# Optimization experiments

Hardware: AMD Instinct MI355X
Metric: run time of the kernel (lower is better)

## Reference

```python
import jax, jax.numpy as jnp
import numpy as np

N = 40000   # entities
R = 200     # relations
T = 250000  # train edges (one direction)
E = 2 * T + N  # fwd + reverse + self-loops
D0, D = 100, 200   # init_emb_size, embedding_dim (= gc1_emb_size)
C, K = 128, 5      # conv channels, kernel size
B = 2048           # query batch
EPS = 1e-5


def setup_inputs() -> dict:
    key = jax.random.key(0)
    ks = jax.random.split(key, 24)
    def nrm(k, shape, s=0.05):
        return jax.random.normal(k, shape, jnp.float32) * s
    def bnp(k, dim):  # [gamma, beta, running_mean, running_var] stacked -> [4, dim]
        g = 1.0 + nrm(k, (dim,))
        b = nrm(jax.random.fold_in(k, 1), (dim,))
        m = nrm(jax.random.fold_in(k, 2), (dim,))
        v = 1.0 + 0.1 * jax.random.uniform(jax.random.fold_in(k, 3), (dim,), jnp.float32)
        return jnp.stack([g, b, m, v])
    inp = dict(
        src=jax.random.randint(ks[0], (E,), 0, N),
        dst=jax.random.randint(ks[1], (E,), 0, N),
        all_edge_type=jax.random.randint(ks[2], (E,), 0, R + 1),
        e1=jax.random.randint(ks[3], (B, 1), 0, N),
        rel=jax.random.randint(ks[4], (B, 1), 0, R),
        entity_id=jnp.arange(N),
        emb_e_w=nrm(ks[5], (N, D0), 0.1).at[0].set(0.0),   # padding_idx=0
        emb_rel_w=nrm(ks[6], (R, D), 0.1).at[0].set(0.0),
        w2=nrm(ks[7], (D0, D)), b2=nrm(ks[8], (D,)),
        alpha2=nrm(ks[9], (R + 1, 1)).at[0].set(0.0),
        w3=nrm(ks[10], (D, D)), b3=nrm(ks[11], (D,)),
        alpha3=nrm(ks[12], (R + 1, 1)).at[0].set(0.0),
        bn3=bnp(ks[13], D), bn4=bnp(ks[14], D),
        bn0=bnp(ks[15], 2), bn1=bnp(ks[16], C), bn2=bnp(ks[17], D),
        conv_w=nrm(ks[18], (C, 2, K)), conv_b=nrm(ks[19], (C,)),
        fc_w=nrm(ks[20], (D, D * C), 0.01), fc_b=nrm(ks[21], (D,)),
    )
    return inp


def _bn(x, p):  # eval-mode BatchNorm1d over last dim; p: [4, dim]
    g, b, m, v = p[0], p[1], p[2], p[3]
    return g * (x - m) * jax.lax.rsqrt(v + EPS) + b


def _bn_ch(x, p):  # x: [B, C, L]; normalize over channel dim
    g, b, m, v = (p[i][None, :, None] for i in range(4))
    return g * (x - m) * jax.lax.rsqrt(v + EPS) + b


def _gcn(x, w, b, alpha, src, dst, alp_types, alp_types_t, n):
    feats = x @ w                                   # [N, out]
    alp = alpha[alp_types] + alpha[alp_types_t]     # [E, 1]
    out = jax.ops.segment_sum(feats[src] * alp, dst, num_segments=n)
    return out + b


def reference(src, dst, all_edge_type, e1, rel, entity_id,
              emb_e_w, emb_rel_w, w2, b2, alpha2, w3, b3, alpha3,
              bn3, bn4, bn0, bn1, bn2, conv_w, conv_b, fc_w, fc_b):
    n = entity_id.shape[0]
    t = (all_edge_type.shape[0] - n) // 2
    # transpose edge types: [reverse, forward, self-loops]
    types_t = jnp.concatenate([all_edge_type[t:2 * t], all_edge_type[:t], all_edge_type[2 * t:]])

    x = emb_e_w[entity_id]                                   # [N, D0]
    x = _gcn(x, w2, b2, alpha2, src, dst, all_edge_type, types_t, n)
    x = jnp.tanh(_bn(x, bn3))                                # dropout: eval -> identity
    x = _gcn(x, w3, b3, alpha3, src, dst, all_edge_type, types_t, n)
    x = jnp.tanh(_bn(x, bn4))                                # final_bn + final_act
    e_all = x                                                # [N, D]

    e1_emb = e_all[e1]                                       # [B, 1, D]
    rel_emb = emb_rel_w[rel]                                 # [B, 1, D]
    h = jnp.concatenate([e1_emb, rel_emb], axis=1)           # [B, 2, D]
    h = _bn_ch(h, bn0)
    h = jax.lax.conv_general_dilated(h, conv_w, (1,), [(K // 2, K // 2)],
                                     dimension_numbers=('NCH', 'OIH', 'NCH'))
    h = h + conv_b[None, :, None]                            # [B, C, D]
    h = jax.nn.relu(_bn_ch(h, bn1))
    h = h.reshape(h.shape[0], -1)                            # [B, C*D]
    h = h @ fc_w.T + fc_b                                    # [B, D]
    h = jax.nn.relu(_bn(h, bn2))
    return jax.nn.sigmoid(h @ e_all.T)                       # [B, N]
```

## Files before the change

kernel.cpp:

```cpp
#include <hip/hip_runtime.h>
#include <math.h>

#define NENT 40000
#define NTE  250000
#define NE   540000
#define DIM0 100
#define DIM  200
#define CCH  128
#define BQ   2048
#define FCK  25600
#define EPSB 1e-5f
#define KPAD 224
#define EMBS 104
#define NSPLIT 32
#define KSEG 800

typedef float f32x4 __attribute__((ext_vector_type(4)));
typedef _Float16 h8 __attribute__((ext_vector_type(8)));
typedef _Float16 h4 __attribute__((ext_vector_type(4)));

#if defined(__has_builtin)
#if __has_builtin(__builtin_amdgcn_global_load_lds)
#define HAVE_GLL 1
#endif
#endif

__device__ __forceinline__ void gload_lds16(const void* g, void* l) {
#ifdef HAVE_GLL
    __builtin_amdgcn_global_load_lds((const __attribute__((address_space(1))) unsigned int*)g,
                                     (__attribute__((address_space(3))) unsigned int*)l, 16, 0, 0);
#else
    *(uint4*)l = *(const uint4*)g;
#endif
}

__global__ void k_hist(const int* __restrict__ dst, int* __restrict__ deg) {
    int e = blockIdx.x * 256 + threadIdx.x;
    if (e < NE) atomicAdd(&deg[dst[e]], 1);
}

__global__ __launch_bounds__(1024) void k_scan(const int* __restrict__ deg,
        int* __restrict__ rowptr, int* __restrict__ cursor) {
    __shared__ int sums[1024];
    int t = threadIdx.x;
    int base = t * 40;
    int local[40];
    int s = 0;
    #pragma unroll
    for (int i = 0; i < 40; i++) {
        int idx = base + i;
        int v = (idx < NENT) ? deg[idx] : 0;
        local[i] = s;
        s += v;
    }
    sums[t] = s;
    __syncthreads();
    #pragma unroll
    for (int off = 1; off < 1024; off <<= 1) {
        int add = (t >= off) ? sums[t - off] : 0;
        __syncthreads();
        sums[t] += add;
        __syncthreads();
    }
    int prefix = (t == 0) ? 0 : sums[t - 1];
    #pragma unroll
    for (int i = 0; i < 40; i++) {
        int idx = base + i;
        if (idx < NENT) {
            int p = prefix + local[i];
            rowptr[idx] = p;
            cursor[idx] = p;
        }
    }
    if (t == 1023) rowptr[NENT] = prefix + s;
}

__global__ void k_scatter(const int* __restrict__ src, const int* __restrict__ dst,
                          const int* __restrict__ aet, const float* __restrict__ a2t,
                          const float* __restrict__ a3t, int* __restrict__ cursor,
                          int* __restrict__ ssrc, float* __restrict__ sa1,
                          float* __restrict__ sa2) {
    int e = blockIdx.x * 256 + threadIdx.x;
    if (e >= NE) return;
    int tt = (e < NTE) ? e + NTE : (e < 2 * NTE ? e - NTE : e);
    int t0 = aet[e], t1 = aet[tt];
    int pos = atomicAdd(&cursor[dst[e]], 1);
    ssrc[pos] = src[e];
    sa1[pos] = a2t[t0] + a2t[t1];
    sa2[pos] = a3t[t0] + a3t[t1];
}

template<int NL, int NPADL, int SS, int OS>
__global__ __launch_bounds__(256) void k_agg_raw(const int* __restrict__ rowptr,
        const int* __restrict__ ssrc, const float* __restrict__ sa,
        const _Float16* __restrict__ srcd, _Float16* __restrict__ outd) {
    int w = threadIdx.x >> 6, l = threadIdx.x & 63;
    int row = blockIdx.x * 4 + w;
    int beg = rowptr[row], end = rowptr[row + 1];
    bool act = l < NL;
    int col = l * 4;
    float sx = 0.f, sy = 0.f, sz = 0.f, sw = 0.f;
    int i = beg;
    for (; i + 4 <= end; i += 4) {
        int i0 = ssrc[i], i1 = ssrc[i + 1], i2 = ssrc[i + 2], i3 = ssrc[i + 3];
        float a0 = sa[i], a1 = sa[i + 1], a2 = sa[i + 2], a3 = sa[i + 3];
        if (act) {
            h4 v0 = *(const h4*)(srcd + (long)i0 * SS + col);
            h4 v1 = *(const h4*)(srcd + (long)i1 * SS + col);
            h4 v2 = *(const h4*)(srcd + (long)i2 * SS + col);
            h4 v3 = *(const h4*)(srcd + (long)i3 * SS + col);
            sx += a0 * (float)v0[0] + a1 * (float)v1[0] + a2 * (float)v2[0] + a3 * (float)v3[0];
            sy += a0 * (float)v0[1] + a1 * (float)v1[1] + a2 * (float)v2[1] + a3 * (float)v3[1];
            sz += a0 * (float)v0[2] + a1 * (float)v1[2] + a2 * (float)v2[2] + a3 * (float)v3[2];
            sw += a0 * (float)v0[3] + a1 * (float)v1[3] + a2 * (float)v2[3] + a3 * (float)v3[3];
        }
    }
    for (; i < end; i++) {
        int i0 = ssrc[i];
        float a0 = sa[i];
        if (act) {
            h4 v0 = *(const h4*)(srcd + (long)i0 * SS + col);
            sx += a0 * (float)v0[0]; sy += a0 * (float)v0[1];
            sz += a0 * (float)v0[2]; sw += a0 * (float)v0[3];
        }
    }
    if (act) {
        h4 o = { (_Float16)sx, (_Float16)sy, (_Float16)sz, (_Float16)sw };
        *(h4*)(outd + (long)row * OS + col) = o;
    } else if (l < NPADL) {
        h4 z = { (_Float16)0.f, (_Float16)0.f, (_Float16)0.f, (_Float16)0.f };
        *(h4*)(outd + (long)row * OS + col) = z;
    }
}

__global__ void k_pack_emb(const float* __restrict__ emb, const int* __restrict__ ent,
                           _Float16* __restrict__ o) {
    long i = (long)blockIdx.x * 256 + threadIdx.x;
    if (i >= (long)NENT * 13) return;
    long m = i / 13;
    int k0 = (int)(i % 13) * 8;
    h8 h = {};
    const float* p = emb + (long)ent[m] * DIM0 + k0;
    #pragma unroll
    for (int j = 0; j < 8; j++)
        if (k0 + j < DIM0) h[j] = (_Float16)p[j];
    *(h8*)(o + m * EMBS + k0) = h;
}

__global__ void k_pack_B16(const float* __restrict__ w, _Float16* __restrict__ bf,
                           int kin, int kpad, int nrows) {
    int i = blockIdx.x * 256 + threadIdx.x;
    if (i >= nrows * kpad) return;
    int k = i % kpad, n = i / kpad;
    bf[i] = (k < kin && n < DIM) ? (_Float16)w[(long)k * DIM + n] : (_Float16)0.f;
}

__global__ void k_hq(const int* __restrict__ e1, const int* __restrict__ rel,
                     const _Float16* __restrict__ ef, const float* __restrict__ embrel,
                     const float* __restrict__ bn0, float* __restrict__ hq) {
    int i = blockIdx.x * 256 + threadIdx.x;
    if (i >= BQ * 2 * DIM) return;
    int d = i % DIM, c = (i / DIM) & 1, b = i / (2 * DIM);
    float val = (c == 0) ? (float)ef[(long)e1[b] * KPAD + d]
                         : embrel[(long)rel[b] * DIM + d];
    float g = bn0[c], be = bn0[2 + c], m = bn0[4 + c], v = bn0[6 + c];
    hq[i] = g * (val - m) * rsqrtf(v + EPSB) + be;
}

__global__ void k_pack_fcw(const float* __restrict__ w, _Float16* __restrict__ wf) {
    long i = (long)blockIdx.x * 256 + threadIdx.x;
    if (i >= (long)208 * (FCK / 8)) return;
    int n = (int)(i / (FCK / 8));
    long k0 = (i % (FCK / 8)) * 8;
    h8 h = {};
    if (n < DIM) {
        const float* p = w + (long)n * FCK + k0;
        #pragma unroll
        for (int j = 0; j < 8; j++) h[j] = (_Float16)p[j];
    }
    *(h8*)(wf + (long)n * FCK + k0) = h;
}

template<int NT>
__global__ __launch_bounds__(256) void k_gemm16f(
        const _Float16* __restrict__ A, const _Float16* __restrict__ B,
        const float* __restrict__ bias, const float* __restrict__ bn,
        _Float16* __restrict__ C, int kpad, int ostride) {
    int w = threadIdx.x >> 6, l = threadIdx.x & 63;
    long m0 = (long)blockIdx.x * 64 + w * 16;
    long arow = m0 + (l & 15);
    int kg = (l >> 4) * 8;
    const _Float16* ap = A + arow * kpad + kg;
    f32x4 acc[NT];
    #pragma unroll
    for (int i = 0; i < NT; i++) acc[i] = (f32x4){0.f, 0.f, 0.f, 0.f};
    for (int kb = 0; kb < kpad; kb += 32) {
        h8 a = *(const h8*)(ap + kb);
        #pragma unroll
        for (int nt = 0; nt < NT; nt++) {
            h8 b = *(const h8*)(B + (long)(nt * 16 + (l & 15)) * kpad + kb + kg);
            acc[nt] = __builtin_amdgcn_mfma_f32_16x16x32_f16(a, b, acc[nt], 0, 0, 0);
        }
    }
    long rowo = m0 + (l >> 4) * 4;
    #pragma unroll
    for (int nt = 0; nt < NT; nt++) {
        int col = nt * 16 + (l & 15);
        if (col < ostride) {
            _Float16 vals[4];
            if (col < DIM) {
                float g = bn[col], be = bn[DIM + col], m = bn[2 * DIM + col],
                      v = bn[3 * DIM + col], bb = bias[col];
                float sc = g * rsqrtf(v + EPSB);
                #pragma unroll
                for (int rr = 0; rr < 4; rr++)
                    vals[rr] = (_Float16)tanhf(sc * (acc[nt][rr] + bb - m) + be);
            } else {
                #pragma unroll
                for (int rr = 0; rr < 4; rr++) vals[rr] = (_Float16)0.f;
            }
            #pragma unroll
            for (int rr = 0; rr < 4; rr++)
                C[(rowo + rr) * ostride + col] = vals[rr];
        }
    }
}

__global__ __launch_bounds__(256) void k_conv2(const float* __restrict__ hq,
        const float* __restrict__ convw, const float* __restrict__ convb,
        const float* __restrict__ bn1, _Float16* __restrict__ hc) {
    __shared__ float hql[400];
    __shared__ float cwl[1280];
    __shared__ float scs[128], shs[128];
    int bl = blockIdx.x;
    int t = threadIdx.x;
    long b = bl;
    for (int i = t; i < 400; i += 256) hql[i] = hq[b * 400 + i];
    for (int i = t; i < 1280; i += 256) cwl[i] = convw[i];
    if (t < 128) {
        float g = bn1[t], be = bn1[CCH + t], m = bn1[2 * CCH + t], v = bn1[3 * CCH + t];
        float s = g * rsqrtf(v + EPSB);
        scs[t] = s;
        shs[t] = be - m * s + s * convb[t];
    }
    __syncthreads();
    int c = t >> 1, half = t & 1, p0 = half * 100;
    float cw[10];
    #pragma unroll
    for (int k = 0; k < 10; k++) cw[k] = cwl[c * 10 + k];
    float sc_ = scs[c], sh_ = shs[c];
    long obase = (long)bl * FCK + c * DIM + p0;
    for (int pc = 0; pc < 100; pc += 4) {
        float w0[8], w1[8];
        #pragma unroll
        for (int j = 0; j < 8; j++) {
            int pp = p0 + pc - 2 + j;
            bool ok = (pp >= 0 && pp < DIM);
            w0[j] = ok ? hql[pp] : 0.f;
            w1[j] = ok ? hql[DIM + pp] : 0.f;
        }
        h4 o;
        #pragma unroll
        for (int j = 0; j < 4; j++) {
            float s = 0.f;
            #pragma unroll
            for (int k = 0; k < 5; k++) s += w0[j + k] * cw[k] + w1[j + k] * cw[5 + k];
            o[j] = (_Float16)fmaxf(sc_ * s + sh_, 0.f);
        }
        *(h4*)&hc[obase + pc] = o;
    }
}

__global__ __launch_bounds__(256) void k_fc2(
        const _Float16* __restrict__ A, const _Float16* __restrict__ B,
        float* __restrict__ fcsum) {
    __shared__ __align__(16) _Float16 ldsB[2][6656];
    int bid = blockIdx.y * 8 + blockIdx.x;
    int wsw = (bid & 7) * 128 + (bid >> 3);
    int mb = wsw & 31, split = wsw >> 5;
    int t = threadIdx.x;
    int w = t >> 6, l = t & 63;
    int kbase = split * KSEG;
    long arow = mb * 64 + w * 16 + (l & 15);
    int kg = (l >> 4) * 8;
    const _Float16* ahp = A + arow * FCK + kbase + kg;

    #pragma unroll
    for (int i = 0; i < 4; i++) {
        int u = i * 256 + t;
        if (u < 832) {
            int r = u >> 2, kc = u & 3;
            gload_lds16(B + (long)r * FCK + kbase + kc * 8, &ldsB[0][u * 8]);
        }
    }
    h8 aN = *(const h8*)(ahp);

    f32x4 acc[13];
    #pragma unroll
    for (int i = 0; i < 13; i++) acc[i] = (f32x4){0.f, 0.f, 0.f, 0.f};

    int buf = 0;
    for (int ks = 0; ks < 25; ks++) {
        __syncthreads();
        if (ks + 1 < 25) {
            int knext = kbase + (ks + 1) * 32;
            #pragma unroll
            for (int i = 0; i < 4; i++) {
                int u = i * 256 + t;
                if (u < 832) {
                    int r = u >> 2, kc = u & 3;
                    gload_lds16(B + (long)r * FCK + knext + kc * 8, &ldsB[buf ^ 1][u * 8]);
                }
            }
        }
        h8 aC = aN;
        if (ks + 1 < 25) aN = *(const h8*)(ahp + (ks + 1) * 32);
        const _Float16* b_base = &ldsB[buf][(l & 15) * 32 + kg];
        #pragma unroll
        for (int nt = 0; nt < 13; nt++) {
            h8 b = *(const h8*)(b_base + nt * 512);
            acc[nt] = __builtin_amdgcn_mfma_f32_16x16x32_f16(aC, b, acc[nt], 0, 0, 0);
        }
        buf ^= 1;
    }
    long rowo = mb * 64 + w * 16 + (l >> 4) * 4;
    #pragma unroll
    for (int nt = 0; nt < 13; nt++) {
        int col = nt * 16 + (l & 15);
        if (col < DIM) {
            #pragma unroll
            for (int rr = 0; rr < 4; rr++)
                unsafeAtomicAdd(&fcsum[(rowo + rr) * DIM + col], acc[nt][rr]);
        }
    }
}

__global__ void k_fcreduce(const float* __restrict__ fcsum, const float* __restrict__ fcb,
                           const float* __restrict__ bn2, _Float16* __restrict__ h3) {
    int i = blockIdx.x * 256 + threadIdx.x;
    if (i >= BQ * KPAD) return;
    int j = i % KPAD, b = i / KPAD;
    _Float16 o = (_Float16)0.f;
    if (j < DIM) {
        float s = fcsum[(long)b * DIM + j] + fcb[j];
        float g = bn2[j], be = bn2[DIM + j], m = bn2[2 * DIM + j], v = bn2[3 * DIM + j];
        s = g * (s - m) * rsqrtf(v + EPSB) + be;
        o = (_Float16)fmaxf(s, 0.f);
    }
    h3[i] = o;
}

__global__ __launch_bounds__(256) void k_mfma_final(
        const _Float16* __restrict__ A, const _Float16* __restrict__ B,
        float* __restrict__ out) {
    __shared__ float tl[4][32][68];
    int bid = blockIdx.y * 8 + blockIdx.x;
    int wsw = (bid & 7) * 625 + (bid >> 3);
    int mbb = wsw & 7, nbb = wsw >> 3;
    int w = threadIdx.x >> 6, l = threadIdx.x & 63;
    int n0 = nbb * 64;
    int m0 = mbb * 256 + w * 64;
    int lr = l & 15;
    int kb = (l >> 4) * 8;
    const _Float16* aph = A + (long)(m0 + lr) * KPAD + kb;
    const _Float16* bph = B + (long)(n0 + lr) * KPAD + kb;
    h8 ac[4], bc[4], an[4], bn_[4];
    #pragma unroll
    for (int x = 0; x < 4; x++) {
        ac[x] = *(const h8*)(aph + (long)x * 16 * KPAD);
        bc[x] = *(const h8*)(bph + (long)x * 16 * KPAD);
    }
    f32x4 acc[4][4];
    #pragma unroll
    for (int i = 0; i < 4; i++)
        #pragma unroll
        for (int j = 0; j < 4; j++) acc[i][j] = (f32x4){0.f, 0.f, 0.f, 0.f};
    for (int kt = 0; kt < 7; kt++) {
        int ko = kt * 32 + 32;
        if (kt < 6) {
            #pragma unroll
            for (int x = 0; x < 4; x++) {
                an[x]  = *(const h8*)(aph + (long)x * 16 * KPAD + ko);
                bn_[x] = *(const h8*)(bph + (long)x * 16 * KPAD + ko);
            }
        }
        #pragma unroll
        for (int mt = 0; mt < 4; mt++)
            #pragma unroll
            for (int nt = 0; nt < 4; nt++)
                acc[mt][nt] = __builtin_amdgcn_mfma_f32_16x16x32_f16(ac[mt], bc[nt], acc[mt][nt], 0, 0, 0);
        if (kt < 6) {
            #pragma unroll
            for (int x = 0; x < 4; x++) { ac[x] = an[x]; bc[x] = bn_[x]; }
        }
    }
    #pragma unroll
    for (int hh = 0; hh < 2; hh++) {
        #pragma unroll
        for (int mt2 = 0; mt2 < 2; mt2++) {
            int mt = hh * 2 + mt2;
            #pragma unroll
            for (int nt = 0; nt < 4; nt++)
                #pragma unroll
                for (int r = 0; r < 4; r++)
                    tl[w][mt2 * 16 + (l >> 4) * 4 + r][nt * 16 + lr] = acc[mt][nt][r];
        }
        #pragma unroll
        for (int i = 0; i < 8; i++) {
            int rr = i * 4 + (l >> 4);
            f32x4 v = *(const f32x4*)&tl[w][rr][lr * 4];
            f32x4 o;
            o.x = __builtin_amdgcn_rcpf(1.f + __expf(-v.x));
            o.y = __builtin_amdgcn_rcpf(1.f + __expf(-v.y));
            o.z = __builtin_amdgcn_rcpf(1.f + __expf(-v.z));
            o.w = __builtin_amdgcn_rcpf(1.f + __expf(-v.w));
            long row = m0 + hh * 32 + rr;
            __builtin_nontemporal_store(o, (f32x4*)&out[row * NENT + n0 + lr * 4]);
        }
    }
}

extern "C" void kernel_launch(void* const* d_in, const int* in_sizes, int n_in,
                              void* d_out, int out_size, void* d_ws, size_t ws_size,
                              hipStream_t stream) {
    (void)in_sizes; (void)n_in; (void)out_size; (void)ws_size;
    const int* src      = (const int*)d_in[0];
    const int* dst      = (const int*)d_in[1];
    const int* aet      = (const int*)d_in[2];
    const int* e1       = (const int*)d_in[3];
    const int* rel      = (const int*)d_in[4];
    const int* entity   = (const int*)d_in[5];
    const float* emb_e  = (const float*)d_in[6];
    const float* embrel = (const float*)d_in[7];
    const float* w2     = (const float*)d_in[8];
    const float* b2     = (const float*)d_in[9];
    const float* alpha2 = (const float*)d_in[10];
    const float* w3     = (const float*)d_in[11];
    const float* b3     = (const float*)d_in[12];
    const float* alpha3 = (const float*)d_in[13];
    const float* bn3    = (const float*)d_in[14];
    const float* bn4    = (const float*)d_in[15];
    const float* bn0    = (const float*)d_in[16];
    const float* bn1    = (const float*)d_in[17];
    const float* bn2    = (const float*)d_in[18];
    const float* convw  = (const float*)d_in[19];
    const float* convb  = (const float*)d_in[20];
    const float* fcw    = (const float*)d_in[21];
    const float* fcb    = (const float*)d_in[22];
    float* out = (float*)d_out;
    float* ws = (float*)d_ws;

    _Float16* emb16 = (_Float16*)ws;
    _Float16* aggE  = (_Float16*)(ws + 3000000);
    _Float16* x1_f  = (_Float16*)(ws + 6000000);
    _Float16* aggX  = (_Float16*)(ws + 11000000);
    _Float16* e_f   = (_Float16*)(ws + 16000000);
    _Float16* fcw_f = (_Float16*)(ws + 21000000);
    _Float16* hc_f  = (_Float16*)(ws + 24000000);
    int*   deg    = (int*)(ws + 51000000);
    int*   rowptr = (int*)(ws + 51050000);
    int*   cursor = (int*)(ws + 51100000);
    int*   ssrc   = (int*)(ws + 51200000);
    float* sa1    = ws + 51800000;
    float* sa2    = ws + 52400000;
    float* fcsum  = ws + 53000000;
    float* hq     = ws + 53500000;
    _Float16* h3_f  = (_Float16*)(ws + 54400000);
    _Float16* w2t_f = (_Float16*)(ws + 54700000);
    _Float16* w3t_f = (_Float16*)(ws + 54750000);

    hipMemsetAsync(deg, 0, NENT * 4, stream);
    k_hist<<<(NE + 255) / 256, 256, 0, stream>>>(dst, deg);
    k_scan<<<1, 1024, 0, stream>>>(deg, rowptr, cursor);
    k_scatter<<<(NE + 255) / 256, 256, 0, stream>>>(src, dst, aet, alpha2, alpha3,
                                                    cursor, ssrc, sa1, sa2);

    k_pack_emb<<<(NENT * 13 + 255) / 256, 256, 0, stream>>>(emb_e, entity, emb16);
    k_pack_B16<<<(208 * 128 + 255) / 256, 256, 0, stream>>>(w2, w2t_f, DIM0, 128, 208);
    k_pack_B16<<<(224 * KPAD + 255) / 256, 256, 0, stream>>>(w3, w3t_f, DIM, KPAD, 224);

    k_agg_raw<26, 32, EMBS, 128><<<NENT / 4, 256, 0, stream>>>(rowptr, ssrc, sa1,
                                                               emb16, aggE);
    k_gemm16f<13><<<NENT / 64, 256, 0, stream>>>(aggE, w2t_f, b2, bn3, x1_f, 128, DIM);

    k_agg_raw<50, 56, DIM, KPAD><<<NENT / 4, 256, 0, stream>>>(rowptr, ssrc, sa2,
                                                               x1_f, aggX);
    k_gemm16f<14><<<NENT / 64, 256, 0, stream>>>(aggX, w3t_f, b3, bn4, e_f, KPAD, KPAD);

    k_hq<<<(BQ * 2 * DIM + 255) / 256, 256, 0, stream>>>(e1, rel, e_f, embrel, bn0, hq);
    k_pack_fcw<<<(int)(((long)208 * (FCK / 8) + 255) / 256), 256, 0, stream>>>(fcw, fcw_f);

    hipMemsetAsync(fcsum, 0, (size_t)BQ * DIM * 4, stream);
    k_conv2<<<BQ, 256, 0, stream>>>(hq, convw, convb, bn1, hc_f);
    k_fc2<<<dim3(8, 128), 256, 0, stream>>>(hc_f, fcw_f, fcsum);
    k_fcreduce<<<(BQ * KPAD + 255) / 256, 256, 0, stream>>>(fcsum, fcb, bn2, h3_f);

    k_mfma_final<<<dim3(8, NENT / 64), 256, 0, stream>>>(h3_f, e_f, out);
}
```

Measured before the change: 543.9 us.

## Fuse conv1d+BN+ReLU into FC split-K GEMM, computing A tiles on the fly

Removes the separate conv kernel that wrote the 2048x25600 fp16 conv output (about 100MB) and re-read it in the FC GEMM. The FC kernel now computes each 64x32 A tile directly from the fp16 query embeddings held in registers, writes it to LDS, and stages B through registers instead of async global-to-LDS loads. The query input is also stored as fp16. In exchange, conv arithmetic is recomputed inside the GEMM loop, each step adds a second barrier, and the B double-buffer is replaced by register prefetching, which may lower overlap.

```diff
diff --git a/kernel.cpp b/kernel.cpp
--- a/kernel.cpp
+++ b/kernel.cpp
@@ -12,27 +12,10 @@
 #define EPSB 1e-5f
 #define KPAD 224
 #define EMBS 104
-#define NSPLIT 32
-#define KSEG 800
 
 typedef float f32x4 __attribute__((ext_vector_type(4)));
 typedef _Float16 h8 __attribute__((ext_vector_type(8)));
 typedef _Float16 h4 __attribute__((ext_vector_type(4)));
-
-#if defined(__has_builtin)
-#if __has_builtin(__builtin_amdgcn_global_load_lds)
-#define HAVE_GLL 1
-#endif
-#endif
-
-__device__ __forceinline__ void gload_lds16(const void* g, void* l) {
-#ifdef HAVE_GLL
-    __builtin_amdgcn_global_load_lds((const __attribute__((address_space(1))) unsigned int*)g,
-                                     (__attribute__((address_space(3))) unsigned int*)l, 16, 0, 0);
-#else
-    *(uint4*)l = *(const uint4*)g;
-#endif
-}
 
 __global__ void k_hist(const int* __restrict__ dst, int* __restrict__ deg) {
     int e = blockIdx.x * 256 + threadIdx.x;
@@ -155,16 +138,16 @@
     bf[i] = (k < kin && n < DIM) ? (_Float16)w[(long)k * DIM + n] : (_Float16)0.f;
 }
 
-__global__ void k_hq(const int* __restrict__ e1, const int* __restrict__ rel,
-                     const _Float16* __restrict__ ef, const float* __restrict__ embrel,
-                     const float* __restrict__ bn0, float* __restrict__ hq) {
+__global__ void k_hq16(const int* __restrict__ e1, const int* __restrict__ rel,
+                       const _Float16* __restrict__ ef, const float* __restrict__ embrel,
+                       const float* __restrict__ bn0, _Float16* __restrict__ hq) {
     int i = blockIdx.x * 256 + threadIdx.x;
     if (i >= BQ * 2 * DIM) return;
     int d = i % DIM, c = (i / DIM) & 1, b = i / (2 * DIM);
     float val = (c == 0) ? (float)ef[(long)e1[b] * KPAD + d]
                          : embrel[(long)rel[b] * DIM + d];
     float g = bn0[c], be = bn0[2 + c], m = bn0[4 + c], v = bn0[6 + c];
-    hq[i] = g * (val - m) * rsqrtf(v + EPSB) + be;
+    hq[i] = (_Float16)(g * (val - m) * rsqrtf(v + EPSB) + be);
 }
 
 __global__ void k_pack_fcw(const float* __restrict__ w, _Float16* __restrict__ wf) {
@@ -226,102 +209,111 @@
     }
 }
 
-__global__ __launch_bounds__(256) void k_conv2(const float* __restrict__ hq,
-        const float* __restrict__ convw, const float* __restrict__ convb,
-        const float* __restrict__ bn1, _Float16* __restrict__ hc) {
-    __shared__ float hql[400];
-    __shared__ float cwl[1280];
-    __shared__ float scs[128], shs[128];
-    int bl = blockIdx.x;
-    int t = threadIdx.x;
-    long b = bl;
-    for (int i = t; i < 400; i += 256) hql[i] = hq[b * 400 + i];
-    for (int i = t; i < 1280; i += 256) cwl[i] = convw[i];
-    if (t < 128) {
-        float g = bn1[t], be = bn1[CCH + t], m = bn1[2 * CCH + t], v = bn1[3 * CCH + t];
-        float s = g * rsqrtf(v + EPSB);
-        scs[t] = s;
-        shs[t] = be - m * s + s * convb[t];
-    }
-    __syncthreads();
-    int c = t >> 1, half = t & 1, p0 = half * 100;
-    float cw[10];
-    #pragma unroll
-    for (int k = 0; k < 10; k++) cw[k] = cwl[c * 10 + k];
-    float sc_ = scs[c], sh_ = shs[c];
-    long obase = (long)bl * FCK + c * DIM + p0;
-    for (int pc = 0; pc < 100; pc += 4) {
-        float w0[8], w1[8];
-        #pragma unroll
-        for (int j = 0; j < 8; j++) {
-            int pp = p0 + pc - 2 + j;
-            bool ok = (pp >= 0 && pp < DIM);
-            w0[j] = ok ? hql[pp] : 0.f;
-            w1[j] = ok ? hql[DIM + pp] : 0.f;
-        }
-        h4 o;
-        #pragma unroll
-        for (int j = 0; j < 4; j++) {
-            float s = 0.f;
-            #pragma unroll
-            for (int k = 0; k < 5; k++) s += w0[j + k] * cw[k] + w1[j + k] * cw[5 + k];
-            o[j] = (_Float16)fmaxf(sc_ * s + sh_, 0.f);
-        }
-        *(h4*)&hc[obase + pc] = o;
-    }
-}
-
-__global__ __launch_bounds__(256) void k_fc2(
-        const _Float16* __restrict__ A, const _Float16* __restrict__ B,
-        float* __restrict__ fcsum) {
-    __shared__ __align__(16) _Float16 ldsB[2][6656];
+__global__ __launch_bounds__(256) void k_convfc(
+        const _Float16* __restrict__ hq16, const float* __restrict__ convw,
+        const float* __restrict__ convb, const float* __restrict__ bn1,
+        const _Float16* __restrict__ B, float* __restrict__ fcsum) {
+    __shared__ _Float16 ldsA[64][40];
+    __shared__ _Float16 ldsB[208][40];
+    __shared__ float cwl[4][12];
     int bid = blockIdx.y * 8 + blockIdx.x;
     int wsw = (bid & 7) * 128 + (bid >> 3);
     int mb = wsw & 31, split = wsw >> 5;
     int t = threadIdx.x;
     int w = t >> 6, l = t & 63;
-    int kbase = split * KSEG;
-    long arow = mb * 64 + w * 16 + (l & 15);
-    int kg = (l >> 4) * 8;
-    const _Float16* ahp = A + arow * FCK + kbase + kg;
-
-    #pragma unroll
-    for (int i = 0; i < 4; i++) {
-        int u = i * 256 + t;
-        if (u < 832) {
-            int r = u >> 2, kc = u & 3;
-            gload_lds16(B + (long)r * FCK + kbase + kc * 8, &ldsB[0][u * 8]);
-        }
-    }
-    h8 aN = *(const h8*)(ahp);
+    int kbase = split * 800;
+    int c0 = split * 4;
+    if (t < 40) cwl[t / 10][t % 10] = convw[(c0 + t / 10) * 10 + t % 10];
+    if (t < 4) {
+        int c = c0 + t;
+        float g = bn1[c], be = bn1[CCH + c], m = bn1[2 * CCH + c], v = bn1[3 * CCH + c];
+        float s = g * rsqrtf(v + EPSB);
+        cwl[t][10] = s;
+        cwl[t][11] = be - m * s + s * convb[c];
+    }
+    __syncthreads();
+
+    int r = t >> 2, q = t & 3;
+    const _Float16* hrow = hq16 + (long)(mb * 64 + r) * 400;
+
+    h8 z = {};
+    h8 v0a, v1a, v2a, v0b, v1b, v2b;
+    {
+        int p = q * 8;
+        v0a = (p >= 8) ? *(const h8*)(hrow + p - 8) : z;
+        v1a = *(const h8*)(hrow + p);
+        v2a = (p + 8 < DIM) ? *(const h8*)(hrow + p + 8) : z;
+        v0b = (p >= 8) ? *(const h8*)(hrow + DIM + p - 8) : z;
+        v1b = *(const h8*)(hrow + DIM + p);
+        v2b = (p + 8 < DIM) ? *(const h8*)(hrow + DIM + p + 8) : z;
+    }
+    h8 bR[4];
+    #pragma unroll
+    for (int i2 = 0; i2 < 4; i2++) {
+        int u = i2 * 256 + t;
+        bR[i2] = (u < 832) ? *(const h8*)(B + (long)(u >> 2) * FCK + kbase + (u & 3) * 8) : z;
+    }
 
     f32x4 acc[13];
     #pragma unroll
     for (int i = 0; i < 13; i++) acc[i] = (f32x4){0.f, 0.f, 0.f, 0.f};
 
-    int buf = 0;
     for (int ks = 0; ks < 25; ks++) {
+        int off = ks * 32 + q * 8;
+        int cl = off / 200;
+        float cwv[12];
+        #pragma unroll
+        for (int k2 = 0; k2 < 12; k2++) cwv[k2] = cwl[cl][k2];
+        float wa[12], wb[12];
+        wa[0] = (float)v0a[6]; wa[1] = (float)v0a[7];
+        wb[0] = (float)v0b[6]; wb[1] = (float)v0b[7];
+        #pragma unroll
+        for (int m2 = 0; m2 < 8; m2++) {
+            wa[2 + m2] = (float)v1a[m2];
+            wb[2 + m2] = (float)v1b[m2];
+        }
+        wa[10] = (float)v2a[0]; wa[11] = (float)v2a[1];
+        wb[10] = (float)v2b[0]; wb[11] = (float)v2b[1];
+        h8 aOut;
+        #pragma unroll
+        for (int j = 0; j < 8; j++) {
+            float s = 0.f;
+            #pragma unroll
+            for (int kk = 0; kk < 5; kk++)
+                s += wa[j + kk] * cwv[kk] + wb[j + kk] * cwv[5 + kk];
+            aOut[j] = (_Float16)fmaxf(cwv[10] * s + cwv[11], 0.f);
+        }
+        *(h8*)&ldsA[r][q * 8] = aOut;
+        #pragma unroll
+        for (int i2 = 0; i2 < 4; i2++) {
+            int u = i2 * 256 + t;
+            if (u < 832) *(h8*)&ldsB[u >> 2][(u & 3) * 8] = bR[i2];
+        }
         __syncthreads();
         if (ks + 1 < 25) {
+            int off1 = (ks + 1) * 32 + q * 8;
+            int cl1 = off1 / 200;
+            int p1 = off1 - cl1 * 200;
+            v0a = (p1 >= 8) ? *(const h8*)(hrow + p1 - 8) : z;
+            v1a = *(const h8*)(hrow + p1);
+            v2a = (p1 + 8 < DIM) ? *(const h8*)(hrow + p1 + 8) : z;
+            v0b = (p1 >= 8) ? *(const h8*)(hrow + DIM + p1 - 8) : z;
+            v1b = *(const h8*)(hrow + DIM + p1);
+            v2b = (p1 + 8 < DIM) ? *(const h8*)(hrow + DIM + p1 + 8) : z;
             int knext = kbase + (ks + 1) * 32;
             #pragma unroll
-            for (int i = 0; i < 4; i++) {
-                int u = i * 256 + t;
-                if (u < 832) {
-                    int r = u >> 2, kc = u & 3;
-                    gload_lds16(B + (long)r * FCK + knext + kc * 8, &ldsB[buf ^ 1][u * 8]);
-                }
+            for (int i2 = 0; i2 < 4; i2++) {
+                int u = i2 * 256 + t;
+                if (u < 832) bR[i2] = *(const h8*)(B + (long)(u >> 2) * FCK + knext + (u & 3) * 8);
             }
         }
-        h8 aC = aN;
-        if (ks + 1 < 25) aN = *(const h8*)(ahp + (ks + 1) * 32);
-        const _Float16* b_base = &ldsB[buf][(l & 15) * 32 + kg];
+        h8 a = *(const h8*)&ldsA[w * 16 + (l & 15)][(l >> 4) * 8];
         #pragma unroll
         for (int nt = 0; nt < 13; nt++) {
-            h8 b = *(const h8*)(b_base + nt * 512);
-            acc[nt] = __builtin_amdgcn_mfma_f32_16x16x32_f16(aC, b, acc[nt], 0, 0, 0);
-        }
-        buf ^= 1;
+            h8 b = *(const h8*)&ldsB[nt * 16 + (l & 15)][(l >> 4) * 8];
+            acc[nt] = __builtin_amdgcn_mfma_f32_16x16x32_f16(a, b, acc[nt], 0, 0, 0);
+        }
+        __syncthreads();
     }
     long rowo = mb * 64 + w * 16 + (l >> 4) * 4;
     #pragma unroll
@@ -456,7 +448,7 @@
     _Float16* aggX  = (_Float16*)(ws + 11000000);
     _Float16* e_f   = (_Float16*)(ws + 16000000);
     _Float16* fcw_f = (_Float16*)(ws + 21000000);
-    _Float16* hc_f  = (_Float16*)(ws + 24000000);
+    _Float16* hq16  = (_Float16*)(ws + 24000000);
     int*   deg    = (int*)(ws + 51000000);
     int*   rowptr = (int*)(ws + 51050000);
     int*   cursor = (int*)(ws + 51100000);
@@ -464,7 +456,6 @@
     float* sa1    = ws + 51800000;
     float* sa2    = ws + 52400000;
     float* fcsum  = ws + 53000000;
-    float* hq     = ws + 53500000;
     _Float16* h3_f  = (_Float16*)(ws + 54400000);
     _Float16* w2t_f = (_Float16*)(ws + 54700000);
     _Float16* w3t_f = (_Float16*)(ws + 54750000);
@@ -487,12 +478,11 @@
                                                                x1_f, aggX);
     k_gemm16f<14><<<NENT / 64, 256, 0, stream>>>(aggX, w3t_f, b3, bn4, e_f, KPAD, KPAD);
 
-    k_hq<<<(BQ * 2 * DIM + 255) / 256, 256, 0, stream>>>(e1, rel, e_f, embrel, bn0, hq);
+    k_hq16<<<(BQ * 2 * DIM + 255) / 256, 256, 0, stream>>>(e1, rel, e_f, embrel, bn0, hq16);
     k_pack_fcw<<<(int)(((long)208 * (FCK / 8) + 255) / 256), 256, 0, stream>>>(fcw, fcw_f);
 
     hipMemsetAsync(fcsum, 0, (size_t)BQ * DIM * 4, stream);
-    k_conv2<<<BQ, 256, 0, stream>>>(hq, convw, convb, bn1, hc_f);
-    k_fc2<<<dim3(8, 128), 256, 0, stream>>>(hc_f, fcw_f, fcsum);
+    k_convfc<<<dim3(8, 128), 256, 0, stream>>>(hq16, convw, convb, bn1, fcw_f, fcsum);
     k_fcreduce<<<(BQ * KPAD + 255) / 256, 256, 0, stream>>>(fcsum, fcb, bn2, h3_f);
 
     k_mfma_final<<<dim3(8, NENT / 64), 256, 0, stream>>>(h3_f, e_f, out);
```

After: 518.3 us. -4.7%, faster.
